# Kernel tuning notes

Hardware: AMD Instinct MI355X
Metric: run time of the kernel (lower is better)

## Reference

```python
import jax, jax.numpy as jnp
import numpy as np

B, LM, LX, D = 16, 1024, 1024, 768


def setup_inputs() -> dict:
    key = jax.random.key(0)
    k1, k2, k3, k4 = jax.random.split(key, 4)
    main = jax.random.normal(k1, (B, LM, D), dtype=jnp.float32)
    x = jax.random.normal(k2, (B, LX, D), dtype=jnp.float32)
    # keras 'uniform' init ~ U(-0.05, 0.05); scale to keep activations sane
    W = jax.random.uniform(k3, (D, D), dtype=jnp.float32, minval=-0.05, maxval=0.05)
    w = jax.random.uniform(k4, (2 * D, 1), dtype=jnp.float32, minval=-0.05, maxval=0.05)
    return {"main": main, "x": x, "W": W, "w": w}


def reference(main, x, W, w):
    # bilinear co-attention scores: (main @ W) . x^T -> (B, LM, LX)
    proj = jnp.einsum('bmd,de->bme', main, W)            # (B, LM, D)
    scores = jnp.einsum('bme,bne->bmn', proj, x)         # (B, LM, LX) -- no softmax in original
    A = jnp.einsum('bmn,bnd->bmd', scores, x)            # attended features (B, LM, D)
    s = main - A
    m = main * A
    outputs = jnp.concatenate([s, m], axis=-1)           # (B, LM, 2D)
    beta = jnp.einsum('bmk,k->bm', outputs, w[:, 0])     # (B, LM) -- raw, no softmax
    pooled = jnp.einsum('bm,bmk->bk', beta, outputs)     # weighted-sum pooling (B, 2D)
    return pooled
```

## Files before the change

kernel.cpp:

```cpp
#include <hip/hip_runtime.h>

constexpr int kB  = 16;
constexpr int kLM = 1024;
constexpr int kLX = 1024;
constexpr int kD  = 768;

using short8 = __attribute__((ext_vector_type(8))) short;
using f32x4  = __attribute__((ext_vector_type(4))) float;

__device__ __forceinline__ unsigned short f2bf(float f) {
    unsigned u = __float_as_uint(f);
    u = (u + 0x7FFF + ((u >> 16) & 1)) >> 16;
    return (unsigned short)u;
}
__device__ __forceinline__ float bf2f(unsigned short h) {
    return __uint_as_float(((unsigned)h) << 16);
}

__global__ __launch_bounds__(256) void transpose_cvt_kernel(
    const float* __restrict__ x, unsigned short* __restrict__ xT) {
    __shared__ float tile[64][65];
    const int b  = blockIdx.z;
    const int l0 = blockIdx.x * 64;
    const int d0 = blockIdx.y * 64;
    const int t  = threadIdx.x;
    const int tx = t & 15, ty = t >> 4;
    const float* xb = x + ((size_t)b * kLX + l0) * kD + d0;
#pragma unroll
    for (int p = 0; p < 4; ++p) {
        int r = p * 16 + ty;
        float4 v = *(const float4*)(xb + (size_t)r * kD + tx * 4);
        *(float4*)&tile[r][tx * 4] = v;
    }
    __syncthreads();
    unsigned short* xTb = xT + ((size_t)b * kD + d0) * kLX + l0;
#pragma unroll
    for (int p = 0; p < 4; ++p) {
        int dr = p * 16 + ty;
        ushort4 o;
        o.x = f2bf(tile[tx * 4 + 0][dr]);
        o.y = f2bf(tile[tx * 4 + 1][dr]);
        o.z = f2bf(tile[tx * 4 + 2][dr]);
        o.w = f2bf(tile[tx * 4 + 3][dr]);
        *(ushort4*)(xTb + (size_t)dr * kLX + tx * 4) = o;
    }
}

__global__ __launch_bounds__(256) void cvt_bf16_kernel(
    const float* __restrict__ in, unsigned short* __restrict__ out, int n4) {
    int i = blockIdx.x * blockDim.x + threadIdx.x;
    if (i < n4) {
        float4 v = ((const float4*)in)[i];
        ushort4 o;
        o.x = f2bf(v.x); o.y = f2bf(v.y); o.z = f2bf(v.z); o.w = f2bf(v.w);
        ((ushort4*)out)[i] = o;
    }
}

constexpr int LDT = 40;
__global__ __launch_bounds__(256) void gemm_nt_bf16_kernel(
    const unsigned short* __restrict__ A, const unsigned short* __restrict__ B,
    unsigned short* __restrict__ C, int M, int N, int K,
    long sA, long sB, long sC) {
    __shared__ unsigned short Asm[128 * LDT];
    __shared__ unsigned short Bsm[128 * LDT];
    const int b  = blockIdx.z;
    const int i0 = blockIdx.x * 128;
    const int j0 = blockIdx.y * 128;
    const int t    = threadIdx.x;
    const int wave = t >> 6, lane = t & 63;
    const int wr = (wave >> 1) * 64, wc = (wave & 1) * 64;
    const int quad = lane >> 4, l15 = lane & 15;

    const unsigned short* Ab = A + (size_t)b * sA + (size_t)i0 * K;
    const unsigned short* Bb = B + (size_t)b * sB + (size_t)j0 * K;

    const int srow = t >> 2;
    const int sseg = t & 3;

    f32x4 acc[4][4];
    const f32x4 z = {0.f, 0.f, 0.f, 0.f};
#pragma unroll
    for (int i = 0; i < 4; ++i)
#pragma unroll
        for (int j = 0; j < 4; ++j) acc[i][j] = z;

    for (int k0 = 0; k0 < K; k0 += 32) {
        float4 a0 = *(const float4*)(Ab + (size_t)srow * K + k0 + sseg * 8);
        float4 a1 = *(const float4*)(Ab + (size_t)(srow + 64) * K + k0 + sseg * 8);
        float4 b0 = *(const float4*)(Bb + (size_t)srow * K + k0 + sseg * 8);
        float4 b1 = *(const float4*)(Bb + (size_t)(srow + 64) * K + k0 + sseg * 8);
        __syncthreads();
        *(float4*)(Asm + srow * LDT + sseg * 8)        = a0;
        *(float4*)(Asm + (srow + 64) * LDT + sseg * 8) = a1;
        *(float4*)(Bsm + srow * LDT + sseg * 8)        = b0;
        *(float4*)(Bsm + (srow + 64) * LDT + sseg * 8) = b1;
        __syncthreads();
        short8 af[4], bg[4];
#pragma unroll
        for (int i = 0; i < 4; ++i)
            af[i] = *(const short8*)(Asm + (wr + i * 16 + l15) * LDT + quad * 8);
#pragma unroll
        for (int j = 0; j < 4; ++j)
            bg[j] = *(const short8*)(Bsm + (wc + j * 16 + l15) * LDT + quad * 8);
#pragma unroll
        for (int i = 0; i < 4; ++i)
#pragma unroll
            for (int j = 0; j < 4; ++j)
                acc[i][j] = __builtin_amdgcn_mfma_f32_16x16x32_bf16(
                    af[i], bg[j], acc[i][j], 0, 0, 0);
    }

    unsigned short* Cb = C + (size_t)b * sC + (size_t)(i0 + wr) * N + j0 + wc;
#pragma unroll
    for (int i = 0; i < 4; ++i)
#pragma unroll
        for (int j = 0; j < 4; ++j)
#pragma unroll
            for (int r = 0; r < 4; ++r)
                Cb[(size_t)(i * 16 + quad * 4 + r) * N + j * 16 + l15] =
                    f2bf(acc[i][j][r]);
}

__global__ __launch_bounds__(256) void pool_kernel(
    const float* __restrict__ mainp, const unsigned short* __restrict__ Aout,
    const float* __restrict__ w, float* __restrict__ out) {
    const int b     = blockIdx.y;
    const int chunk = blockIdx.x;
    const int wave  = threadIdx.x >> 6, lane = threadIdx.x & 63;
    float w1[12], w2[12], ps[12], pm[12];
#pragma unroll
    for (int s = 0; s < 12; ++s) {
        w1[s] = w[s * 64 + lane];
        w2[s] = w[kD + s * 64 + lane];
        ps[s] = 0.f; pm[s] = 0.f;
    }
    for (int rr = 0; rr < 16; ++rr) {
        const int row = chunk * 64 + rr * 4 + wave;
        const float* mr = mainp + ((size_t)b * kLM + row) * kD;
        const unsigned short* ar = Aout + ((size_t)b * kLM + row) * kD;
        float sv[12], mv[12], acc = 0.f;
#pragma unroll
        for (int s = 0; s < 12; ++s) {
            float m_ = mr[s * 64 + lane];
            float a_ = bf2f(ar[s * 64 + lane]);
            sv[s] = m_ - a_;
            mv[s] = m_ * a_;
            acc += sv[s] * w1[s] + mv[s] * w2[s];
        }
#pragma unroll
        for (int off = 32; off; off >>= 1) acc += __shfl_xor(acc, off);
#pragma unroll
        for (int s = 0; s < 12; ++s) { ps[s] += acc * sv[s]; pm[s] += acc * mv[s]; }
    }
    float* ob = out + (size_t)b * 2 * kD;
#pragma unroll
    for (int s = 0; s < 12; ++s) {
        atomicAdd(&ob[s * 64 + lane], ps[s]);
        atomicAdd(&ob[kD + s * 64 + lane], pm[s]);
    }
}

extern "C" void kernel_launch(void* const* d_in, const int* in_sizes, int n_in,
                              void* d_out, int out_size, void* d_ws, size_t ws_size,
                              hipStream_t stream) {
    const float* mainp = (const float*)d_in[0];
    const float* x     = (const float*)d_in[1];
    const float* W     = (const float*)d_in[2];
    const float* w     = (const float*)d_in[3];
    float* out = (float*)d_out;

    char* p = (char*)d_ws;
    unsigned short* xT    = (unsigned short*)p; p += (size_t)kB * kD * kLX * 2;
    unsigned short* mainb = (unsigned short*)p; p += (size_t)kB * kLM * kD * 2;
    unsigned short* Wb    = (unsigned short*)p; p += (size_t)kD * kD * 2;
    unsigned short* G     = (unsigned short*)p; p += (size_t)kB * kD * kD * 2;
    unsigned short* Mt    = (unsigned short*)p; p += (size_t)kB * kD * kD * 2;
    unsigned short* Ao    = (unsigned short*)p; p += (size_t)kB * kLM * kD * 2;

    hipMemsetAsync(out, 0, (size_t)kB * 2 * kD * sizeof(float), stream);

    transpose_cvt_kernel<<<dim3(kLX / 64, kD / 64, kB), 256, 0, stream>>>(x, xT);
    {
        int n4 = kB * kLM * kD / 4;
        cvt_bf16_kernel<<<(n4 + 255) / 256, 256, 0, stream>>>(mainp, mainb, n4);
        n4 = kD * kD / 4;
        cvt_bf16_kernel<<<(n4 + 255) / 256, 256, 0, stream>>>(W, Wb, n4);
    }
    gemm_nt_bf16_kernel<<<dim3(kD / 128, kD / 128, kB), 256, 0, stream>>>(
        xT, xT, G, kD, kD, kLX, (long)kD * kLX, (long)kD * kLX, (long)kD * kD);
    gemm_nt_bf16_kernel<<<dim3(kD / 128, kD / 128, kB), 256, 0, stream>>>(
        G, Wb, Mt, kD, kD, kD, (long)kD * kD, 0L, (long)kD * kD);
    gemm_nt_bf16_kernel<<<dim3(kLM / 128, kD / 128, kB), 256, 0, stream>>>(
        mainb, Mt, Ao, kLM, kD, kD, (long)kLM * kD, (long)kD * kD, (long)kLM * kD);
    pool_kernel<<<dim3(kLM / 64, kB), 256, 0, stream>>>(mainp, Ao, w, out);
}
```

Measured before the change: 260.8 us.

## Load GEMM tiles directly into LDS with global_load_lds and XOR swizzle

```diff
diff --git a/kernel.cpp b/kernel.cpp
--- a/kernel.cpp
+++ b/kernel.cpp
@@ -15,6 +15,12 @@
 }
 __device__ __forceinline__ float bf2f(unsigned short h) {
     return __uint_as_float(((unsigned)h) << 16);
+}
+
+__device__ __forceinline__ void gl_lds16(const unsigned short* g, unsigned short* l) {
+    auto gp = (const __attribute__((address_space(1))) unsigned int*)g;
+    auto lp = (__attribute__((address_space(3))) unsigned int*)l;
+    __builtin_amdgcn_global_load_lds(gp, lp, 16, 0, 0);
 }
 
 __global__ __launch_bounds__(256) void transpose_cvt_kernel(
@@ -57,13 +63,12 @@
     }
 }
 
-constexpr int LDT = 40;
 __global__ __launch_bounds__(256) void gemm_nt_bf16_kernel(
     const unsigned short* __restrict__ A, const unsigned short* __restrict__ B,
     unsigned short* __restrict__ C, int M, int N, int K,
     long sA, long sB, long sC) {
-    __shared__ unsigned short Asm[128 * LDT];
-    __shared__ unsigned short Bsm[128 * LDT];
+    __shared__ unsigned short Asm[128 * 32];
+    __shared__ unsigned short Bsm[128 * 32];
     const int b  = blockIdx.z;
     const int i0 = blockIdx.x * 128;
     const int j0 = blockIdx.y * 128;
@@ -75,8 +80,21 @@
     const unsigned short* Ab = A + (size_t)b * sA + (size_t)i0 * K;
     const unsigned short* Bb = B + (size_t)b * sB + (size_t)j0 * K;
 
-    const int srow = t >> 2;
-    const int sseg = t & 3;
+    const int c0 = wave * 64 + lane;
+    const int c1 = 256 + wave * 64 + lane;
+    auto chunk_off = [&](int c) -> size_t {
+        int sr = c >> 3, s = c & 7;
+        int tt = s ^ (sr & 7);
+        int r  = sr * 2 + (tt >> 2);
+        int q  = tt & 3;
+        return (size_t)r * K + q * 8;
+    };
+    const size_t off0 = chunk_off(c0);
+    const size_t off1 = chunk_off(c1);
+
+    const int sfr = ((l15 & 1) * 4 + quad) ^ ((l15 >> 1) & 7);
+    const unsigned short* aP = Asm + ((wr >> 1) * 64 + (l15 >> 1) * 64 + sfr * 8);
+    const unsigned short* bP = Bsm + ((wc >> 1) * 64 + (l15 >> 1) * 64 + sfr * 8);
 
     f32x4 acc[4][4];
     const f32x4 z = {0.f, 0.f, 0.f, 0.f};
@@ -86,23 +104,17 @@
         for (int j = 0; j < 4; ++j) acc[i][j] = z;
 
     for (int k0 = 0; k0 < K; k0 += 32) {
-        float4 a0 = *(const float4*)(Ab + (size_t)srow * K + k0 + sseg * 8);
-        float4 a1 = *(const float4*)(Ab + (size_t)(srow + 64) * K + k0 + sseg * 8);
-        float4 b0 = *(const float4*)(Bb + (size_t)srow * K + k0 + sseg * 8);
-        float4 b1 = *(const float4*)(Bb + (size_t)(srow + 64) * K + k0 + sseg * 8);
         __syncthreads();
-        *(float4*)(Asm + srow * LDT + sseg * 8)        = a0;
-        *(float4*)(Asm + (srow + 64) * LDT + sseg * 8) = a1;
-        *(float4*)(Bsm + srow * LDT + sseg * 8)        = b0;
-        *(float4*)(Bsm + (srow + 64) * LDT + sseg * 8) = b1;
+        gl_lds16(Ab + off0 + k0, Asm + c0 * 8);
+        gl_lds16(Ab + off1 + k0, Asm + c1 * 8);
+        gl_lds16(Bb + off0 + k0, Bsm + c0 * 8);
+        gl_lds16(Bb + off1 + k0, Bsm + c1 * 8);
         __syncthreads();
         short8 af[4], bg[4];
 #pragma unroll
-        for (int i = 0; i < 4; ++i)
-            af[i] = *(const short8*)(Asm + (wr + i * 16 + l15) * LDT + quad * 8);
-#pragma unroll
-        for (int j = 0; j < 4; ++j)
-            bg[j] = *(const short8*)(Bsm + (wc + j * 16 + l15) * LDT + quad * 8);
+        for (int i = 0; i < 4; ++i) af[i] = *(const short8*)(aP + i * 512);
+#pragma unroll
+        for (int j = 0; j < 4; ++j) bg[j] = *(const short8*)(bP + j * 512);
 #pragma unroll
         for (int i = 0; i < 4; ++i)
 #pragma unroll
```

Result: no change. 256.1 us (-1.8%).

## Load GEMM fragments directly from global memory and fuse the fp32 main conversion

Applied to the files above, without the earlier changes.

```diff
diff --git a/kernel.cpp b/kernel.cpp
--- a/kernel.cpp
+++ b/kernel.cpp
@@ -15,6 +15,12 @@
 }
 __device__ __forceinline__ float bf2f(unsigned short h) {
     return __uint_as_float(((unsigned)h) << 16);
+}
+__device__ __forceinline__ short8 cvt8(float4 lo, float4 hi) {
+    union { short8 v; unsigned short u[8]; } o;
+    o.u[0] = f2bf(lo.x); o.u[1] = f2bf(lo.y); o.u[2] = f2bf(lo.z); o.u[3] = f2bf(lo.w);
+    o.u[4] = f2bf(hi.x); o.u[5] = f2bf(hi.y); o.u[6] = f2bf(hi.z); o.u[7] = f2bf(hi.w);
+    return o.v;
 }
 
 __global__ __launch_bounds__(256) void transpose_cvt_kernel(
@@ -46,24 +52,20 @@
     }
 }
 
-__global__ __launch_bounds__(256) void cvt_bf16_kernel(
-    const float* __restrict__ in, unsigned short* __restrict__ out, int n4) {
-    int i = blockIdx.x * blockDim.x + threadIdx.x;
-    if (i < n4) {
-        float4 v = ((const float4*)in)[i];
-        ushort4 o;
-        o.x = f2bf(v.x); o.y = f2bf(v.y); o.z = f2bf(v.z); o.w = f2bf(v.w);
-        ((ushort4*)out)[i] = o;
-    }
-}
-
-constexpr int LDT = 40;
-__global__ __launch_bounds__(256) void gemm_nt_bf16_kernel(
-    const unsigned short* __restrict__ A, const unsigned short* __restrict__ B,
+__global__ __launch_bounds__(256) void cvt_w_kernel(
+    const float* __restrict__ in, unsigned short* __restrict__ out) {
+    int i = blockIdx.x * 256 + threadIdx.x;
+    float4 v = ((const float4*)in)[i];
+    ushort4 o;
+    o.x = f2bf(v.x); o.y = f2bf(v.y); o.z = f2bf(v.z); o.w = f2bf(v.w);
+    ((ushort4*)out)[i] = o;
+}
+
+template <bool AFP32>
+__global__ __launch_bounds__(256) void gemm_nt_reg(
+    const void* __restrict__ Av, const unsigned short* __restrict__ B,
     unsigned short* __restrict__ C, int M, int N, int K,
     long sA, long sB, long sC) {
-    __shared__ unsigned short Asm[128 * LDT];
-    __shared__ unsigned short Bsm[128 * LDT];
     const int b  = blockIdx.z;
     const int i0 = blockIdx.x * 128;
     const int j0 = blockIdx.y * 128;
@@ -72,11 +74,12 @@
     const int wr = (wave >> 1) * 64, wc = (wave & 1) * 64;
     const int quad = lane >> 4, l15 = lane & 15;
 
-    const unsigned short* Ab = A + (size_t)b * sA + (size_t)i0 * K;
-    const unsigned short* Bb = B + (size_t)b * sB + (size_t)j0 * K;
-
-    const int srow = t >> 2;
-    const int sseg = t & 3;
+    const unsigned short* Ah = AFP32 ? nullptr
+        : (const unsigned short*)Av + (size_t)b * sA + (size_t)(i0 + wr + l15) * K + quad * 8;
+    const float* Af = AFP32
+        ? (const float*)Av + (size_t)b * sA + (size_t)(i0 + wr + l15) * K + quad * 8 : nullptr;
+    const unsigned short* Bh =
+        B + (size_t)b * sB + (size_t)(j0 + wc + l15) * K + quad * 8;
 
     f32x4 acc[4][4];
     const f32x4 z = {0.f, 0.f, 0.f, 0.f};
@@ -85,30 +88,75 @@
 #pragma unroll
         for (int j = 0; j < 4; ++j) acc[i][j] = z;
 
-    for (int k0 = 0; k0 < K; k0 += 32) {
-        float4 a0 = *(const float4*)(Ab + (size_t)srow * K + k0 + sseg * 8);
-        float4 a1 = *(const float4*)(Ab + (size_t)(srow + 64) * K + k0 + sseg * 8);
-        float4 b0 = *(const float4*)(Bb + (size_t)srow * K + k0 + sseg * 8);
-        float4 b1 = *(const float4*)(Bb + (size_t)(srow + 64) * K + k0 + sseg * 8);
-        __syncthreads();
-        *(float4*)(Asm + srow * LDT + sseg * 8)        = a0;
-        *(float4*)(Asm + (srow + 64) * LDT + sseg * 8) = a1;
-        *(float4*)(Bsm + srow * LDT + sseg * 8)        = b0;
-        *(float4*)(Bsm + (srow + 64) * LDT + sseg * 8) = b1;
-        __syncthreads();
-        short8 af[4], bg[4];
-#pragma unroll
-        for (int i = 0; i < 4; ++i)
-            af[i] = *(const short8*)(Asm + (wr + i * 16 + l15) * LDT + quad * 8);
-#pragma unroll
-        for (int j = 0; j < 4; ++j)
-            bg[j] = *(const short8*)(Bsm + (wc + j * 16 + l15) * LDT + quad * 8);
+    short8 ah0[4], ah1[4], bg0[4], bg1[4];
+    float4 af0[4][2], af1[4][2];
+
+    auto loadA0 = [&](int k) {
+#pragma unroll
+        for (int i = 0; i < 4; ++i) {
+            if constexpr (AFP32) {
+                af0[i][0] = *(const float4*)(Af + (size_t)i * 16 * K + k);
+                af0[i][1] = *(const float4*)(Af + (size_t)i * 16 * K + k + 4);
+            } else {
+                ah0[i] = *(const short8*)(Ah + (size_t)i * 16 * K + k);
+            }
+        }
+    };
+    auto loadA1 = [&](int k) {
+#pragma unroll
+        for (int i = 0; i < 4; ++i) {
+            if constexpr (AFP32) {
+                af1[i][0] = *(const float4*)(Af + (size_t)i * 16 * K + k);
+                af1[i][1] = *(const float4*)(Af + (size_t)i * 16 * K + k + 4);
+            } else {
+                ah1[i] = *(const short8*)(Ah + (size_t)i * 16 * K + k);
+            }
+        }
+    };
+    auto loadB0 = [&](int k) {
+#pragma unroll
+        for (int j = 0; j < 4; ++j) bg0[j] = *(const short8*)(Bh + (size_t)j * 16 * K + k);
+    };
+    auto loadB1 = [&](int k) {
+#pragma unroll
+        for (int j = 0; j < 4; ++j) bg1[j] = *(const short8*)(Bh + (size_t)j * 16 * K + k);
+    };
+    auto mfma0 = [&]() {
+        short8 af[4];
+#pragma unroll
+        for (int i = 0; i < 4; ++i)
+            af[i] = AFP32 ? cvt8(af0[i][0], af0[i][1]) : ah0[i];
 #pragma unroll
         for (int i = 0; i < 4; ++i)
 #pragma unroll
             for (int j = 0; j < 4; ++j)
                 acc[i][j] = __builtin_amdgcn_mfma_f32_16x16x32_bf16(
-                    af[i], bg[j], acc[i][j], 0, 0, 0);
+                    af[i], bg0[j], acc[i][j], 0, 0, 0);
+    };
+    auto mfma1 = [&]() {
+        short8 af[4];
+#pragma unroll
+        for (int i = 0; i < 4; ++i)
+            af[i] = AFP32 ? cvt8(af1[i][0], af1[i][1]) : ah1[i];
+#pragma unroll
+        for (int i = 0; i < 4; ++i)
+#pragma unroll
+            for (int j = 0; j < 4; ++j)
+                acc[i][j] = __builtin_amdgcn_mfma_f32_16x16x32_bf16(
+                    af[i], bg1[j], acc[i][j], 0, 0, 0);
+    };
+
+    const int T = K >> 5;
+    loadA0(0); loadB0(0);
+    for (int kt = 0; kt < T; kt += 2) {
+        loadA1((kt + 1) << 5);
+        loadB1((kt + 1) << 5);
+        mfma0();
+        if (kt + 2 < T) {
+            loadA0((kt + 2) << 5);
+            loadB0((kt + 2) << 5);
+        }
+        mfma1();
     }
 
     unsigned short* Cb = C + (size_t)b * sC + (size_t)(i0 + wr) * N + j0 + wc;
@@ -125,9 +173,11 @@
 __global__ __launch_bounds__(256) void pool_kernel(
     const float* __restrict__ mainp, const unsigned short* __restrict__ Aout,
     const float* __restrict__ w, float* __restrict__ out) {
+    __shared__ float red[4][24][64];
     const int b     = blockIdx.y;
     const int chunk = blockIdx.x;
-    const int wave  = threadIdx.x >> 6, lane = threadIdx.x & 63;
+    const int t     = threadIdx.x;
+    const int wave  = t >> 6, lane = t & 63;
     float w1[12], w2[12], ps[12], pm[12];
 #pragma unroll
     for (int s = 0; s < 12; ++s) {
@@ -135,8 +185,9 @@
         w2[s] = w[kD + s * 64 + lane];
         ps[s] = 0.f; pm[s] = 0.f;
     }
-    for (int rr = 0; rr < 16; ++rr) {
-        const int row = chunk * 64 + rr * 4 + wave;
+#pragma unroll
+    for (int rr = 0; rr < 4; ++rr) {
+        const int row = chunk * 16 + rr * 4 + wave;
         const float* mr = mainp + ((size_t)b * kLM + row) * kD;
         const unsigned short* ar = Aout + ((size_t)b * kLM + row) * kD;
         float sv[12], mv[12], acc = 0.f;
@@ -153,11 +204,19 @@
 #pragma unroll
         for (int s = 0; s < 12; ++s) { ps[s] += acc * sv[s]; pm[s] += acc * mv[s]; }
     }
+#pragma unroll
+    for (int s = 0; s < 12; ++s) {
+        red[wave][s][lane]      = ps[s];
+        red[wave][12 + s][lane] = pm[s];
+    }
+    __syncthreads();
     float* ob = out + (size_t)b * 2 * kD;
-#pragma unroll
-    for (int s = 0; s < 12; ++s) {
-        atomicAdd(&ob[s * 64 + lane], ps[s]);
-        atomicAdd(&ob[kD + s * 64 + lane], pm[s]);
+    for (int v = t; v < 24 * 64; v += 256) {
+        const int sl = v >> 6, ln = v & 63;
+        const float sum = red[0][sl][ln] + red[1][sl][ln] +
+                          red[2][sl][ln] + red[3][sl][ln];
+        const int d = (sl < 12) ? sl * 64 + ln : kD + (sl - 12) * 64 + ln;
+        atomicAdd(&ob[d], sum);
     }
 }
 
@@ -171,27 +230,23 @@
     float* out = (float*)d_out;
 
     char* p = (char*)d_ws;
-    unsigned short* xT    = (unsigned short*)p; p += (size_t)kB * kD * kLX * 2;
-    unsigned short* mainb = (unsigned short*)p; p += (size_t)kB * kLM * kD * 2;
-    unsigned short* Wb    = (unsigned short*)p; p += (size_t)kD * kD * 2;
-    unsigned short* G     = (unsigned short*)p; p += (size_t)kB * kD * kD * 2;
-    unsigned short* Mt    = (unsigned short*)p; p += (size_t)kB * kD * kD * 2;
-    unsigned short* Ao    = (unsigned short*)p; p += (size_t)kB * kLM * kD * 2;
+    unsigned short* xT = (unsigned short*)p; p += (size_t)kB * kD * kLX * 2;
+    unsigned short* Wb = (unsigned short*)p; p += (size_t)kD * kD * 2;
+    unsigned short* G  = (unsigned short*)p; p += (size_t)kB * kD * kD * 2;
+    unsigned short* Mt = (unsigned short*)p; p += (size_t)kB * kD * kD * 2;
+    unsigned short* Ao = (unsigned short*)p; p += (size_t)kB * kLM * kD * 2;
 
     hipMemsetAsync(out, 0, (size_t)kB * 2 * kD * sizeof(float), stream);
 
     transpose_cvt_kernel<<<dim3(kLX / 64, kD / 64, kB), 256, 0, stream>>>(x, xT);
-    {
-        int n4 = kB * kLM * kD / 4;
-        cvt_bf16_kernel<<<(n4 + 255) / 256, 256, 0, stream>>>(mainp, mainb, n4);
-        n4 = kD * kD / 4;
-        cvt_bf16_kernel<<<(n4 + 255) / 256, 256, 0, stream>>>(W, Wb, n4);
-    }
-    gemm_nt_bf16_kernel<<<dim3(kD / 128, kD / 128, kB), 256, 0, stream>>>(
+    cvt_w_kernel<<<kD * kD / 1024, 256, 0, stream>>>(W, Wb);
+
+    gemm_nt_reg<false><<<dim3(kD / 128, kD / 128, kB), 256, 0, stream>>>(
         xT, xT, G, kD, kD, kLX, (long)kD * kLX, (long)kD * kLX, (long)kD * kD);
-    gemm_nt_bf16_kernel<<<dim3(kD / 128, kD / 128, kB), 256, 0, stream>>>(
+    gemm_nt_reg<false><<<dim3(kD / 128, kD / 128, kB), 256, 0, stream>>>(
         G, Wb, Mt, kD, kD, kD, (long)kD * kD, 0L, (long)kD * kD);
-    gemm_nt_bf16_kernel<<<dim3(kLM / 128, kD / 128, kB), 256, 0, stream>>>(
-        mainb, Mt, Ao, kLM, kD, kD, (long)kLM * kD, (long)kD * kD, (long)kLM * kD);
-    pool_kernel<<<dim3(kLM / 64, kB), 256, 0, stream>>>(mainp, Ao, w, out);
-}
+    gemm_nt_reg<true><<<dim3(kLM / 128, kD / 128, kB), 256, 0, stream>>>(
+        mainp, Mt, Ao, kLM, kD, kD, (long)kLM * kD, (long)kD * kD, (long)kLM * kD);
+
+    pool_kernel<<<dim3(kLM / 16, kB), 256, 0, stream>>>(mainp, Ao, w, out);
+}
```

New measurement: 424.2 us. 1.63x slower.
